# Kernel optimization log

Hardware: AMD Instinct MI355X
Metric: run time of the kernel (lower is better)

## Reference

```python
import jax, jax.numpy as jnp
import numpy as np
from functools import partial

B, DIN, H, D, HW = 4096, 2048, 1024, 256, 256
MAX_STEPS = 15
STEP = 1.0 / MAX_STEPS
WEIGHT = 1.0


def safe_norm(x):
    # per-sample L2 norm, keepdims, nan-safe at 0
    return jnp.sqrt(jnp.sum(x * x, axis=-1, keepdims=True) + 1e-24)


def setup_inputs() -> dict:
    key = jax.random.key(0)
    ks = jax.random.split(key, 16)
    s = lambda fan: 1.0 / np.sqrt(fan)
    inp = {
        'x_start': jax.random.normal(ks[0], (B, DIN), jnp.float32),
        'x_end': jax.random.normal(ks[1], (B, DIN), jnp.float32),
        'noise_raw': jax.random.normal(ks[2], (B, D), jnp.float32),
        # encoder params
        'W1': jax.random.normal(ks[3], (DIN, H), jnp.float32) * s(DIN),
        'b1': jnp.zeros((H,), jnp.float32),
        'W2': jax.random.normal(ks[4], (H, D), jnp.float32) * s(H),
        'b2': jnp.zeros((D,), jnp.float32),
        # Zermelo wind field params
        'Ww1': jax.random.normal(ks[5], (D, HW), jnp.float32) * s(D),
        'bw1': jnp.zeros((HW,), jnp.float32),
        'Ww2': jax.random.normal(ks[6], (HW, D), jnp.float32) * s(HW),
        'bw2': jnp.zeros((D,), jnp.float32),
        # conformal potential phi params (metric g = exp(phi) I)
        'Wp1': jax.random.normal(ks[7], (D, HW), jnp.float32) * s(D),
        'bp1': jnp.zeros((HW,), jnp.float32),
        'wp2': jax.random.normal(ks[8], (HW,), jnp.float32) * s(HW),
    }
    return inp


def _encode(x, W1, b1, W2, b2):
    return jnp.tanh(x @ W1 + b1) @ W2 + b2  # [B, D]


def _wind(z, Ww1, bw1, Ww2, bw2):
    return jnp.tanh(z @ Ww1 + bw1) @ Ww2 + bw2  # [B, D]


def _grad_phi(x, Wp1, bp1, wp2):
    # phi(x) = wp2 . tanh(x @ Wp1 + bp1); analytic gradient, fully vectorized
    h = jnp.tanh(x @ Wp1 + bp1)          # [B, HW]
    return ((1.0 - h * h) * wp2) @ Wp1.T  # [B, D]


def _accel(x, v, Wp1, bp1, wp2):
    # geodesic spray of conformal metric e^{phi} I:
    # a = -(grad_phi . v) v + 0.5 |v|^2 grad_phi
    g = _grad_phi(x, Wp1, bp1, wp2)
    gv = jnp.sum(g * v, axis=-1, keepdims=True)
    vv = jnp.sum(v * v, axis=-1, keepdims=True)
    return -gv * v + 0.5 * vv * g


def _trace(z0, v0, Wp1, bp1, wp2):
    h = STEP
    acc = partial(_accel, Wp1=Wp1, bp1=bp1, wp2=wp2)

    def step(carry, _):
        x, v = carry
        k1x, k1v = v, acc(x, v)
        k2x, k2v = v + 0.5 * h * k1v, acc(x + 0.5 * h * k1x, v + 0.5 * h * k1v)
        k3x, k3v = v + 0.5 * h * k2v, acc(x + 0.5 * h * k2x, v + 0.5 * h * k2v)
        k4x, k4v = v + h * k3v, acc(x + h * k3x, v + h * k3v)
        xn = x + (h / 6.0) * (k1x + 2 * k2x + 2 * k3x + k4x)
        vn = v + (h / 6.0) * (k1v + 2 * k2v + 2 * k3v + k4v)
        return (xn, vn), xn

    (_, _), xs = jax.lax.scan(step, (z0, v0), None, length=MAX_STEPS)
    return xs  # [MAX_STEPS, B, D] == xs[1:] of the original trace


def reference(x_start, x_end, noise_raw, W1, b1, W2, b2,
              Ww1, bw1, Ww2, bw2, Wp1, bp1, wp2):
    z_s = _encode(x_start, W1, b1, W2, b2)
    z_e = _encode(x_end, W1, b1, W2, b2)
    W_start = _wind(z_s, Ww1, bw1, Ww2, bw2)
    # degenerate-wind fallback: tiny tangent noise (Euclidean manifold -> identity projection)
    noise = noise_raw / (safe_norm(noise_raw) + 1e-12) * 1e-4
    w_norm = safe_norm(W_start)  # [B, 1]
    W_start = jnp.where(w_norm < 1e-5, W_start + noise, W_start)
    xs = _trace(z_s, W_start, Wp1, bp1, wp2)          # [S, B, D]
    dists_sq = jnp.sum((xs - z_e) ** 2, axis=-1)      # [S, B]
    min_dist_sq = jnp.min(dists_sq, axis=0)           # closest approach per sample
    return jnp.mean(min_dist_sq) * WEIGHT
```

## Files before the change

### kernel.cpp

```cpp
#include <hip/hip_runtime.h>
#include <math.h>

typedef short bf8 __attribute__((ext_vector_type(8)));
typedef float f32x4 __attribute__((ext_vector_type(4)));

namespace {

constexpr float H_STEP = 1.0f / 15.0f;

__device__ inline short f2bf(float f) {
  unsigned u = __float_as_uint(f);
  u += 0x7fffu + ((u >> 16) & 1u);
  return (short)(u >> 16);
}

__device__ inline float fast_tanh(float x) {
  const float ax = fabsf(x);
  const float e = __expf(-2.0f * ax);
  const float t = (1.0f - e) * __builtin_amdgcn_rcpf(1.0f + e);
  return copysignf(t, x);
}

__device__ inline float sech2(float x) {
  const float e = __expf(-2.0f * fabsf(x));
  const float r = __builtin_amdgcn_rcpf(1.0f + e);
  return 4.0f * e * r * r;
}

__device__ inline float wave_sum(float v) {
#pragma unroll
  for (int sh = 32; sh > 0; sh >>= 1) v += __shfl_xor(v, sh);
  return v;
}

template <int CTRL>
__device__ inline float dppadd(float v) {
  return v + __int_as_float(__builtin_amdgcn_update_dpp(
                 0, __float_as_int(v), CTRL, 0xF, 0xF, true));
}
__device__ inline float red16(float v) {
  v = dppadd<0x121>(v);
  v = dppadd<0x122>(v);
  v = dppadd<0x124>(v);
  v = dppadd<0x128>(v);
  return v;
}

__device__ inline void async16(const void* g, void* l) {
  __builtin_amdgcn_global_load_lds((__attribute__((address_space(1))) void*)g,
                                   (__attribute__((address_space(3))) void*)l,
                                   16, 0, 0);
}

__global__ __launch_bounds__(256) void prep_all(
    const float* __restrict__ xs, const float* __restrict__ xe,
    const float* __restrict__ W1, const float* __restrict__ W2,
    const float* __restrict__ Ww1, const float* __restrict__ Ww2,
    const float* __restrict__ Wp1, const float* __restrict__ wp2,
    short* __restrict__ XSb, short* __restrict__ W1T, short* __restrict__ W2T,
    short* __restrict__ Ww1T, short* __restrict__ Ww2T,
    short* __restrict__ WpT, short* __restrict__ Wp1s) {
  __shared__ float tile[32][33];
  const int id = blockIdx.x;
  if (id < 2048) {
    const long n = (long)8192 * 2048, half = n >> 1;
    long i = ((long)id * 256 + threadIdx.x) * 4;
    const long stride = (long)2048 * 1024;
    for (; i < n; i += stride) {
      const float* s = (i < half) ? (xs + i) : (xe + (i - half));
      const float4 f = *(const float4*)s;
      ushort4 o;
      o.x = (unsigned short)f2bf(f.x);
      o.y = (unsigned short)f2bf(f.y);
      o.z = (unsigned short)f2bf(f.z);
      o.w = (unsigned short)f2bf(f.w);
      *(ushort4*)(XSb + i) = o;
    }
    return;
  }
  const int tr = threadIdx.x >> 5, tc = threadIdx.x & 31;
  const float* src;
  short* dst;
  int K, N, kt, nt;
  if (id < 4096) {
    src = W1; dst = W1T; K = 2048; N = 1024; kt = (id - 2048) >> 5; nt = (id - 2048) & 31;
  } else if (id < 4352) {
    src = W2; dst = W2T; K = 1024; N = 256; kt = (id - 4096) >> 3; nt = (id - 4096) & 7;
  } else if (id < 4416) {
    src = Ww1; dst = Ww1T; K = 256; N = 256; kt = (id - 4352) >> 3; nt = (id - 4352) & 7;
  } else if (id < 4480) {
    src = Ww2; dst = Ww2T; K = 256; N = 256; kt = (id - 4416) >> 3; nt = (id - 4416) & 7;
  } else if (id < 4544) {
    src = Wp1; dst = WpT; K = 256; N = 256; kt = (id - 4480) >> 3; nt = (id - 4480) & 7;
  } else {
    const int lid = id - 4544;
    const int k0 = (lid >> 3) * 32, n0 = (lid & 7) * 32;
#pragma unroll
    for (int i = 0; i < 32; i += 8) {
      const size_t o = (size_t)(k0 + tr + i) * 256 + n0 + tc;
      Wp1s[o] = f2bf(Wp1[o] * wp2[n0 + tc]);
    }
    return;
  }
  const int k0 = kt * 32, n0 = nt * 32;
#pragma unroll
  for (int i = 0; i < 32; i += 8)
    tile[tr + i][tc] = src[(size_t)(k0 + tr + i) * N + n0 + tc];
  __syncthreads();
#pragma unroll
  for (int i = 0; i < 32; i += 8)
    dst[(size_t)(n0 + tr + i) * K + k0 + tc] = f2bf(tile[tc][tr + i]);
}


__global__ __launch_bounds__(256) void gemm128_tanh(
    const short* __restrict__ A, const short* __restrict__ Bt,
    const float* __restrict__ bias, short* __restrict__ Cb, int M, int N,
    int K) {
  __shared__ __align__(16) short As[2 * 128 * 32];
  __shared__ __align__(16) short Bs[2 * 128 * 32];
  const int tid = threadIdx.x;
  const int w = tid >> 6, lane = tid & 63, q = lane >> 4, l15 = lane & 15;
  const int wm = (w >> 1) * 64, wn = (w & 1) * 64;
  const int m0 = blockIdx.y * 128, n0 = blockIdx.x * 128;
  const f32x4 fzero = {0.0f, 0.0f, 0.0f, 0.0f};
  f32x4 acc[4][4];
#pragma unroll
  for (int mt = 0; mt < 4; ++mt)
#pragma unroll
    for (int nt = 0; nt < 4; ++nt) acc[mt][nt] = fzero;

  for (int k0 = 0; k0 < K; k0 += 64) {
#pragma unroll
    for (int kcb = 0; kcb < 2; ++kcb)
#pragma unroll
      for (int j = 0; j < 2; ++j) {
        const int c = w * 128 + j * 64 + lane;
        async16(A + (size_t)(m0 + (c >> 2)) * K + k0 + kcb * 32 + (c & 3) * 8,
                &As[kcb * 4096 + (w * 128 + j * 64) * 8]);
        async16(Bt + (size_t)(n0 + (c >> 2)) * K + k0 + kcb * 32 + (c & 3) * 8,
                &Bs[kcb * 4096 + (w * 128 + j * 64) * 8]);
      }
    __syncthreads();
#pragma unroll
    for (int kcb = 0; kcb < 2; ++kcb) {
      bf8 af[4], bfr[4];
#pragma unroll
      for (int mt = 0; mt < 4; ++mt)
        af[mt] =
            *(const bf8*)&As[kcb * 4096 + (wm + mt * 16 + l15) * 32 + q * 8];
#pragma unroll
      for (int nt = 0; nt < 4; ++nt)
        bfr[nt] =
            *(const bf8*)&Bs[kcb * 4096 + (wn + nt * 16 + l15) * 32 + q * 8];
#pragma unroll
      for (int mt = 0; mt < 4; ++mt)
#pragma unroll
        for (int nt = 0; nt < 4; ++nt)
          acc[mt][nt] = __builtin_amdgcn_mfma_f32_16x16x32_bf16(
              af[mt], bfr[nt], acc[mt][nt], 0, 0, 0);
    }
    __syncthreads();
  }
#pragma unroll
  for (int mt = 0; mt < 4; ++mt)
#pragma unroll
    for (int nt = 0; nt < 4; ++nt) {
      const int col = n0 + wn + nt * 16 + l15;
      const float bcol = bias[col];
#pragma unroll
      for (int rg = 0; rg < 4; ++rg) {
        const int row = m0 + wm + mt * 16 + q * 4 + rg;
        Cb[(size_t)row * N + col] = f2bf(fast_tanh(acc[mt][nt][rg] + bcol));
      }
    }
}

__global__ __launch_bounds__(256) void gemm64_enc2(
    const short* __restrict__ A, const short* __restrict__ Bt,
    const float* __restrict__ bias, float* __restrict__ Zs,
    float* __restrict__ Ze, int M, int N, int K) {
  __shared__ __align__(16) short As[2 * 64 * 32];
  __shared__ __align__(16) short Bs[2 * 64 * 32];
  const int tid = threadIdx.x;
  const int w = tid >> 6, lane = tid & 63, q = lane >> 4, l15 = lane & 15;
  const int wm = (w >> 1) * 32, wn = (w & 1) * 32;
  const int m0 = blockIdx.y * 64, n0 = blockIdx.x * 64;
  const f32x4 fzero = {0.0f, 0.0f, 0.0f, 0.0f};
  f32x4 acc[2][2];
#pragma unroll
  for (int mt = 0; mt < 2; ++mt)
#pragma unroll
    for (int nt = 0; nt < 2; ++nt) acc[mt][nt] = fzero;

  for (int k0 = 0; k0 < K; k0 += 64) {
    const int c = w * 64 + lane;
#pragma unroll
    for (int kcb = 0; kcb < 2; ++kcb) {
      async16(A + (size_t)(m0 + (c >> 2)) * K + k0 + kcb * 32 + (c & 3) * 8,
              &As[kcb * 2048 + (w * 64) * 8]);
      async16(Bt + (size_t)(n0 + (c >> 2)) * K + k0 + kcb * 32 + (c & 3) * 8,
              &Bs[kcb * 2048 + (w * 64) * 8]);
    }
    __syncthreads();
#pragma unroll
    for (int kcb = 0; kcb < 2; ++kcb) {
      bf8 af[2], bfr[2];
#pragma unroll
      for (int mt = 0; mt < 2; ++mt)
        af[mt] =
            *(const bf8*)&As[kcb * 2048 + (wm + mt * 16 + l15) * 32 + q * 8];
#pragma unroll
      for (int nt = 0; nt < 2; ++nt)
        bfr[nt] =
            *(const bf8*)&Bs[kcb * 2048 + (wn + nt * 16 + l15) * 32 + q * 8];
#pragma unroll
      for (int mt = 0; mt < 2; ++mt)
#pragma unroll
        for (int nt = 0; nt < 2; ++nt)
          acc[mt][nt] = __builtin_amdgcn_mfma_f32_16x16x32_bf16(
              af[mt], bfr[nt], acc[mt][nt], 0, 0, 0);
    }
    __syncthreads();
  }
#pragma unroll
  for (int mt = 0; mt < 2; ++mt)
#pragma unroll
    for (int nt = 0; nt < 2; ++nt) {
      const int col = n0 + wn + nt * 16 + l15;
      const float bcol = bias[col];
#pragma unroll
      for (int rg = 0; rg < 4; ++rg) {
        const int row = m0 + wm + mt * 16 + q * 4 + rg;
        const float val = acc[mt][nt][rg] + bcol;
        if (row < 4096)
          Zs[(size_t)row * N + col] = val;
        else
          Ze[(size_t)(row - 4096) * N + col] = val;
      }
    }
}


__global__ __launch_bounds__(512, 2) void trace_fused(
    const float* __restrict__ Xg, const float* __restrict__ ZEg,
    const float* __restrict__ NZg, const short* __restrict__ WT,
    const short* __restrict__ Wp1s, const short* __restrict__ Ww1T,
    const short* __restrict__ Ww2T, const float* __restrict__ bw1,
    const float* __restrict__ bw2, const float* __restrict__ bp1,
    float* __restrict__ out) {
  constexpr float hs = H_STEP;
  __shared__ __align__(16) short XsL[4096];
  __shared__ __align__(16) short UL[4096];
  __shared__ __align__(16) float gvb[2][16];
  __shared__ __align__(16) float vvb[2][16];
  __shared__ __align__(16) float db[2][16];
  const int tid = threadIdx.x;
  const int w = tid >> 6, lane = tid & 63, q = lane >> 4, l15 = lane & 15;
  const int r0 = blockIdx.x * 16, rb = q * 4;

  if (tid < 16) {
    gvb[0][tid] = 0.0f; gvb[1][tid] = 0.0f;
    vvb[0][tid] = 0.0f; vvb[1][tid] = 0.0f;
    db[0][tid] = 0.0f;  db[1][tid] = 0.0f;
  }

  int cc[2], wadr[2][4], radr[8];
  float bp1c[2], bw1c[2], bw2c[2];
#pragma unroll
  for (int t = 0; t < 2; ++t) {
    const int c = w * 32 + t * 16 + l15;
    cc[t] = c;
    const int kc = c >> 3, cx = kc & 15, cl = c & 7;
#pragma unroll
    for (int rg = 0; rg < 4; ++rg)
      wadr[t][rg] = kc * 128 + ((rb + rg) ^ cx) * 8 + cl;
    bp1c[t] = bp1[c];
    bw1c[t] = bw1[c];
    bw2c[t] = bw2[c];
  }
#pragma unroll
  for (int ks = 0; ks < 8; ++ks) {
    const int kq = ks * 4 + q;
    radr[ks] = (kq * 16 + (l15 ^ (kq & 15))) * 8;
  }
  float x[2][4], ze[2][4], nz[2][4];
#pragma unroll
  for (int t = 0; t < 2; ++t)
#pragma unroll
    for (int rg = 0; rg < 4; ++rg) {
      const size_t off = (size_t)(r0 + rb + rg) * 256 + cc[t];
      x[t][rg] = Xg[off];
      ze[t][rg] = ZEg[off];
      nz[t][rg] = NZg[off];
    }
  const f32x4 fzero = {0.0f, 0.0f, 0.0f, 0.0f};

  float v[2][4];
  {
    bf8 Wf1[2][8], Wf2[2][8];
#pragma unroll
    for (int t = 0; t < 2; ++t)
#pragma unroll
      for (int ks = 0; ks < 8; ++ks) {
        Wf1[t][ks] = *(const bf8*)(Ww1T + cc[t] * 256 + ks * 32 + q * 8);
        Wf2[t][ks] = *(const bf8*)(Ww2T + cc[t] * 256 + ks * 32 + q * 8);
      }
#pragma unroll
    for (int t = 0; t < 2; ++t)
#pragma unroll
      for (int rg = 0; rg < 4; ++rg) XsL[wadr[t][rg]] = f2bf(x[t][rg]);
    __syncthreads();
    bf8 af[8];
#pragma unroll
    for (int ks = 0; ks < 8; ++ks) af[ks] = *(const bf8*)&XsL[radr[ks]];
    f32x4 acc[2];
#pragma unroll
    for (int t = 0; t < 2; ++t) {
      f32x4 a0 = fzero, a1 = fzero;
#pragma unroll
      for (int ks = 0; ks < 8; ks += 2) {
        a0 = __builtin_amdgcn_mfma_f32_16x16x32_bf16(af[ks], Wf1[t][ks], a0,
                                                     0, 0, 0);
        a1 = __builtin_amdgcn_mfma_f32_16x16x32_bf16(af[ks + 1],
                                                     Wf1[t][ks + 1], a1, 0, 0,
                                                     0);
      }
      acc[t] = a0 + a1;
    }
#pragma unroll
    for (int t = 0; t < 2; ++t)
#pragma unroll
      for (int rg = 0; rg < 4; ++rg)
        UL[wadr[t][rg]] = f2bf(fast_tanh(acc[t][rg] + bw1c[t]));
    __syncthreads();
#pragma unroll
    for (int ks = 0; ks < 8; ++ks) af[ks] = *(const bf8*)&UL[radr[ks]];
#pragma unroll
    for (int t = 0; t < 2; ++t) {
      f32x4 a0 = fzero, a1 = fzero;
#pragma unroll
      for (int ks = 0; ks < 8; ks += 2) {
        a0 = __builtin_amdgcn_mfma_f32_16x16x32_bf16(af[ks], Wf2[t][ks], a0,
                                                     0, 0, 0);
        a1 = __builtin_amdgcn_mfma_f32_16x16x32_bf16(af[ks + 1],
                                                     Wf2[t][ks + 1], a1, 0, 0,
                                                     0);
      }
      acc[t] = a0 + a1;
#pragma unroll
      for (int rg = 0; rg < 4; ++rg) v[t][rg] = acc[t][rg] + bw2c[t];
    }
    float pn[4], pm[4];
#pragma unroll
    for (int rg = 0; rg < 4; ++rg) {
      pn[rg] = red16(v[0][rg] * v[0][rg] + v[1][rg] * v[1][rg]);
      pm[rg] = red16(nz[0][rg] * nz[0][rg] + nz[1][rg] * nz[1][rg]);
    }
    if (l15 == 0) {
#pragma unroll
      for (int rg = 0; rg < 4; ++rg) {
        atomicAdd(&gvb[0][rb + rg], pn[rg]);
        atomicAdd(&vvb[0][rb + rg], pm[rg]);
      }
    }
    __syncthreads();
#pragma unroll
    for (int rg = 0; rg < 4; ++rg) {
      const float wn = sqrtf(gvb[0][rb + rg] + 1e-24f);
      const float sc = (wn < 1e-5f)
                           ? 1e-4f / (sqrtf(vvb[0][rb + rg] + 1e-24f) + 1e-12f)
                           : 0.0f;
      v[0][rg] = fmaf(sc, nz[0][rg], v[0][rg]);
      v[1][rg] = fmaf(sc, nz[1][rg], v[1][rg]);
    }
    __syncthreads();
    if (tid < 16) {
      gvb[0][tid] = 0.0f;
      vvb[0][tid] = 0.0f;
    }
    __syncthreads();
  }

  bf8 B1f[2][8], B2f[2][8];
#pragma unroll
  for (int t = 0; t < 2; ++t)
#pragma unroll
    for (int ks = 0; ks < 8; ++ks) {
      B1f[t][ks] = *(const bf8*)(WT + cc[t] * 256 + ks * 32 + q * 8);
      B2f[t][ks] = *(const bf8*)(Wp1s + cc[t] * 256 + ks * 32 + q * 8);
    }
  float ap[2][4], xacc[2][4], vacc[2][4], md[4];
#pragma unroll
  for (int rg = 0; rg < 4; ++rg) {
    ap[0][rg] = 0.0f; ap[1][rg] = 0.0f;
    xacc[0][rg] = 0.0f; xacc[1][rg] = 0.0f;
    vacc[0][rg] = 0.0f; vacc[1][rg] = 0.0f;
    md[rg] = 3.4e38f;
  }
  const float cxv_t[4] = {0.0f, 0.5f * hs, 0.5f * hs, hs};
  const float cxa_t[4] = {0.0f, 0.0f, 0.25f * hs * hs, 0.5f * hs * hs};
  const float cva_t[4] = {0.0f, 0.5f * hs, 0.5f * hs, hs};

#pragma unroll 1
  for (int step = 0; step < 15; ++step) {
#pragma unroll
    for (int st = 0; st < 4; ++st) {
      const int p = st & 1;
      const float cxv = cxv_t[st], cxa = cxa_t[st], cva = cva_t[st];
      float vs[2][4];
#pragma unroll
      for (int t = 0; t < 2; ++t)
#pragma unroll
        for (int rg = 0; rg < 4; ++rg) {
          vs[t][rg] = fmaf(cva, ap[t][rg], v[t][rg]);
          XsL[wadr[t][rg]] =
              f2bf(x[t][rg] + cxv * v[t][rg] + cxa * ap[t][rg]);
        }
      {
        float pv[4];
#pragma unroll
        for (int rg = 0; rg < 4; ++rg)
          pv[rg] = red16(fmaf(vs[0][rg], vs[0][rg], vs[1][rg] * vs[1][rg]));
        if (l15 == 0) {
#pragma unroll
          for (int rg = 0; rg < 4; ++rg) atomicAdd(&vvb[p][rb + rg], pv[rg]);
        }
      }
      __syncthreads();
      if (st == 0 && step > 0) {
        const f32x4 d4 = *(const f32x4*)&db[(step - 1) & 1][rb];
#pragma unroll
        for (int rg = 0; rg < 4; ++rg) md[rg] = fminf(md[rg], d4[rg]);
      }
      bf8 af[8];
#pragma unroll
      for (int ks = 0; ks < 8; ++ks) af[ks] = *(const bf8*)&XsL[radr[ks]];
      f32x4 acc[2];
#pragma unroll
      for (int t = 0; t < 2; ++t) {
        f32x4 a0 = fzero, a1 = fzero;
#pragma unroll
        for (int ks = 0; ks < 8; ks += 2) {
          a0 = __builtin_amdgcn_mfma_f32_16x16x32_bf16(af[ks], B1f[t][ks], a0,
                                                       0, 0, 0);
          a1 = __builtin_amdgcn_mfma_f32_16x16x32_bf16(af[ks + 1],
                                                       B1f[t][ks + 1], a1, 0,
                                                       0, 0);
        }
        acc[t] = a0 + a1;
      }
#pragma unroll
      for (int t = 0; t < 2; ++t)
#pragma unroll
        for (int rg = 0; rg < 4; ++rg)
          UL[wadr[t][rg]] = f2bf(sech2(acc[t][rg] + bp1c[t]));
      if (tid < 16) {
        gvb[p ^ 1][tid] = 0.0f;
        vvb[p ^ 1][tid] = 0.0f;
      }
      __syncthreads();
      if (st == 0 && step > 0 && tid < 16) db[(step - 1) & 1][tid] = 0.0f;
#pragma unroll
      for (int ks = 0; ks < 8; ++ks) af[ks] = *(const bf8*)&UL[radr[ks]];
#pragma unroll
      for (int t = 0; t < 2; ++t) {
        f32x4 a0 = fzero, a1 = fzero;
#pragma unroll
        for (int ks = 0; ks < 8; ks += 2) {
          a0 = __builtin_amdgcn_mfma_f32_16x16x32_bf16(af[ks], B2f[t][ks], a0,
                                                       0, 0, 0);
          a1 = __builtin_amdgcn_mfma_f32_16x16x32_bf16(af[ks + 1],
                                                       B2f[t][ks + 1], a1, 0,
                                                       0, 0);
        }
        acc[t] = a0 + a1;
      }
      {
        float pg[4];
#pragma unroll
        for (int rg = 0; rg < 4; ++rg)
          pg[rg] =
              red16(fmaf(acc[0][rg], vs[0][rg], acc[1][rg] * vs[1][rg]));
        if (l15 == 0) {
#pragma unroll
          for (int rg = 0; rg < 4; ++rg) atomicAdd(&gvb[p][rb + rg], pg[rg]);
        }
      }
      __syncthreads();
      const f32x4 gv4 = *(const f32x4*)&gvb[p][rb];
      const f32x4 vv4 = *(const f32x4*)&vvb[p][rb];
#pragma unroll
      for (int t = 0; t < 2; ++t)
#pragma unroll
        for (int rg = 0; rg < 4; ++rg) {
          const float a = -gv4[rg] * vs[t][rg] + 0.5f * vv4[rg] * acc[t][rg];
          ap[t][rg] = a;
          if (st == 0) {
            xacc[t][rg] = a;
            vacc[t][rg] = a;
          } else if (st < 3) {
            xacc[t][rg] += a;
            vacc[t][rg] += 2.0f * a;
          } else {
            vacc[t][rg] += a;
          }
        }
      if (st == 3) {
        const int sp = step & 1;
        float pd[4];
#pragma unroll
        for (int rg = 0; rg < 4; ++rg) {
          float acc_d = 0.0f;
#pragma unroll
          for (int t = 0; t < 2; ++t) {
            const float xn =
                x[t][rg] + hs * v[t][rg] + (hs * hs / 6.0f) * xacc[t][rg];
            const float vn = v[t][rg] + (hs / 6.0f) * vacc[t][rg];
            x[t][rg] = xn;
            v[t][rg] = vn;
            const float d = xn - ze[t][rg];
            acc_d = fmaf(d, d, acc_d);
          }
          pd[rg] = red16(acc_d);
        }
        if (l15 == 0) {
#pragma unroll
          for (int rg = 0; rg < 4; ++rg) atomicAdd(&db[sp][rb + rg], pd[rg]);
        }
      }
    }
  }
  __syncthreads();
  {
    const f32x4 d4 = *(const f32x4*)&db[14 & 1][rb];
#pragma unroll
    for (int rg = 0; rg < 4; ++rg) md[rg] = fminf(md[rg], d4[rg]);
  }
  if (w == 0 && l15 == 0)
    atomicAdd(out, (md[0] + md[1] + md[2] + md[3]) * (1.0f / 4096.0f));
}

}

extern "C" void kernel_launch(void* const* d_in, const int* in_sizes, int n_in,
                              void* d_out, int out_size, void* d_ws,
                              size_t ws_size, hipStream_t stream) {
  (void)in_sizes; (void)n_in; (void)out_size; (void)ws_size;
  const float* x_start = (const float*)d_in[0];
  const float* x_end = (const float*)d_in[1];
  const float* noise = (const float*)d_in[2];
  const float* W1 = (const float*)d_in[3];
  const float* b1 = (const float*)d_in[4];
  const float* W2 = (const float*)d_in[5];
  const float* b2 = (const float*)d_in[6];
  const float* Ww1 = (const float*)d_in[7];
  const float* bw1 = (const float*)d_in[8];
  const float* Ww2 = (const float*)d_in[9];
  const float* bw2 = (const float*)d_in[10];
  const float* Wp1 = (const float*)d_in[11];
  const float* bp1 = (const float*)d_in[12];
  const float* wp2 = (const float*)d_in[13];
  float* out = (float*)d_out;

  float* Xf = (float*)d_ws;
  float* ZEf = Xf + (size_t)4096 * 256;
  short* XSb = (short*)(ZEf + (size_t)4096 * 256);
  short* H1b = XSb + (size_t)8192 * 2048;
  short* W1T = H1b + (size_t)8192 * 1024;
  short* W2T = W1T + (size_t)1024 * 2048;
  short* Ww1T = W2T + (size_t)256 * 1024;
  short* Ww2T = Ww1T + 65536;
  short* WpT = Ww2T + 65536;
  short* Wp1s = WpT + 65536;

  const dim3 blk(256);

  prep_all<<<4608, blk, 0, stream>>>(x_start, x_end, W1, W2, Ww1, Ww2, Wp1,
                                     wp2, XSb, W1T, W2T, Ww1T, Ww2T, WpT,
                                     Wp1s);
  gemm128_tanh<<<dim3(8, 64), blk, 0, stream>>>(XSb, W1T, b1, H1b, 8192, 1024,
                                                2048);
  gemm64_enc2<<<dim3(4, 128), blk, 0, stream>>>(H1b, W2T, b2, Xf, ZEf, 8192,
                                                256, 1024);
  hipMemsetAsync(d_out, 0, sizeof(float), stream);
  trace_fused<<<256, dim3(512), 0, stream>>>(Xf, ZEf, noise, WpT, Wp1s, Ww1T,
                                             Ww2T, bw1, bw2, bp1, out);
}
```

Before: 325.2 us.

## Halve rows per trace block and double grid; merge reductions and move min update

Each trace_fused block now handles 8 real rows instead of 16. Rows 8-15 are masked padding, and the grid doubles to 512 blocks so more CUs get work during the sequential RK4 loop. The vs/vv reduction moves after the second MFMA and merges with the gv reduction, which removes one red16+atomic phase before the first barrier. The per-step min-distance update moves inside step 3 with an extra barrier, and one redundant barrier is dropped. Half the MFMA work per block is wasted on zero rows, trading compute efficiency for parallelism on 256 CUs.

```diff
diff --git a/kernel.cpp b/kernel.cpp
--- a/kernel.cpp
+++ b/kernel.cpp
@@ -25,12 +25,6 @@
   const float e = __expf(-2.0f * fabsf(x));
   const float r = __builtin_amdgcn_rcpf(1.0f + e);
   return 4.0f * e * r * r;
-}
-
-__device__ inline float wave_sum(float v) {
-#pragma unroll
-  for (int sh = 32; sh > 0; sh >>= 1) v += __shfl_xor(v, sh);
-  return v;
 }
 
 template <int CTRL>
@@ -257,7 +251,8 @@
   __shared__ __align__(16) float db[2][16];
   const int tid = threadIdx.x;
   const int w = tid >> 6, lane = tid & 63, q = lane >> 4, l15 = lane & 15;
-  const int r0 = blockIdx.x * 16, rb = q * 4;
+  const int r0 = blockIdx.x * 8, rb = q * 4;
+  const float valid = (q < 2) ? 1.0f : 0.0f;
 
   if (tid < 16) {
     gvb[0][tid] = 0.0f; gvb[1][tid] = 0.0f;
@@ -289,10 +284,10 @@
   for (int t = 0; t < 2; ++t)
 #pragma unroll
     for (int rg = 0; rg < 4; ++rg) {
-      const size_t off = (size_t)(r0 + rb + rg) * 256 + cc[t];
-      x[t][rg] = Xg[off];
-      ze[t][rg] = ZEg[off];
-      nz[t][rg] = NZg[off];
+      const size_t off = (size_t)(r0 + ((rb + rg) & 7)) * 256 + cc[t];
+      x[t][rg] = Xg[off] * valid;
+      ze[t][rg] = ZEg[off] * valid;
+      nz[t][rg] = NZg[off] * valid;
     }
   const f32x4 fzero = {0.0f, 0.0f, 0.0f, 0.0f};
 
@@ -357,7 +352,7 @@
       pn[rg] = red16(v[0][rg] * v[0][rg] + v[1][rg] * v[1][rg]);
       pm[rg] = red16(nz[0][rg] * nz[0][rg] + nz[1][rg] * nz[1][rg]);
     }
-    if (l15 == 0) {
+    if (l15 == 0 && q < 2) {
 #pragma unroll
       for (int rg = 0; rg < 4; ++rg) {
         atomicAdd(&gvb[0][rb + rg], pn[rg]);
@@ -371,15 +366,14 @@
       const float sc = (wn < 1e-5f)
                            ? 1e-4f / (sqrtf(vvb[0][rb + rg] + 1e-24f) + 1e-12f)
                            : 0.0f;
-      v[0][rg] = fmaf(sc, nz[0][rg], v[0][rg]);
-      v[1][rg] = fmaf(sc, nz[1][rg], v[1][rg]);
+      v[0][rg] = fmaf(sc, nz[0][rg], v[0][rg]) * valid;
+      v[1][rg] = fmaf(sc, nz[1][rg], v[1][rg]) * valid;
     }
     __syncthreads();
     if (tid < 16) {
       gvb[0][tid] = 0.0f;
       vvb[0][tid] = 0.0f;
     }
-    __syncthreads();
   }
 
   bf8 B1f[2][8], B2f[2][8];
@@ -408,31 +402,13 @@
     for (int st = 0; st < 4; ++st) {
       const int p = st & 1;
       const float cxv = cxv_t[st], cxa = cxa_t[st], cva = cva_t[st];
-      float vs[2][4];
 #pragma unroll
       for (int t = 0; t < 2; ++t)
 #pragma unroll
-        for (int rg = 0; rg < 4; ++rg) {
-          vs[t][rg] = fmaf(cva, ap[t][rg], v[t][rg]);
+        for (int rg = 0; rg < 4; ++rg)
           XsL[wadr[t][rg]] =
               f2bf(x[t][rg] + cxv * v[t][rg] + cxa * ap[t][rg]);
-        }
-      {
-        float pv[4];
-#pragma unroll
-        for (int rg = 0; rg < 4; ++rg)
-          pv[rg] = red16(fmaf(vs[0][rg], vs[0][rg], vs[1][rg] * vs[1][rg]));
-        if (l15 == 0) {
-#pragma unroll
-          for (int rg = 0; rg < 4; ++rg) atomicAdd(&vvb[p][rb + rg], pv[rg]);
-        }
-      }
       __syncthreads();
-      if (st == 0 && step > 0) {
-        const f32x4 d4 = *(const f32x4*)&db[(step - 1) & 1][rb];
-#pragma unroll
-        for (int rg = 0; rg < 4; ++rg) md[rg] = fminf(md[rg], d4[rg]);
-      }
       bf8 af[8];
 #pragma unroll
       for (int ks = 0; ks < 8; ++ks) af[ks] = *(const bf8*)&XsL[radr[ks]];
@@ -454,13 +430,12 @@
       for (int t = 0; t < 2; ++t)
 #pragma unroll
         for (int rg = 0; rg < 4; ++rg)
-          UL[wadr[t][rg]] = f2bf(sech2(acc[t][rg] + bp1c[t]));
+          UL[wadr[t][rg]] = f2bf(sech2(acc[t][rg] + bp1c[t]) * valid);
       if (tid < 16) {
         gvb[p ^ 1][tid] = 0.0f;
         vvb[p ^ 1][tid] = 0.0f;
       }
       __syncthreads();
-      if (st == 0 && step > 0 && tid < 16) db[(step - 1) & 1][tid] = 0.0f;
 #pragma unroll
       for (int ks = 0; ks < 8; ++ks) af[ks] = *(const bf8*)&UL[radr[ks]];
 #pragma unroll
@@ -476,15 +451,19 @@
         }
         acc[t] = a0 + a1;
       }
-      {
-        float pg[4];
-#pragma unroll
-        for (int rg = 0; rg < 4; ++rg)
-          pg[rg] =
-              red16(fmaf(acc[0][rg], vs[0][rg], acc[1][rg] * vs[1][rg]));
-        if (l15 == 0) {
-#pragma unroll
-          for (int rg = 0; rg < 4; ++rg) atomicAdd(&gvb[p][rb + rg], pg[rg]);
+      float vs[2][4], pg[4], pv[4];
+#pragma unroll
+      for (int rg = 0; rg < 4; ++rg) {
+        vs[0][rg] = fmaf(cva, ap[0][rg], v[0][rg]);
+        vs[1][rg] = fmaf(cva, ap[1][rg], v[1][rg]);
+        pg[rg] = red16(fmaf(acc[0][rg], vs[0][rg], acc[1][rg] * vs[1][rg]));
+        pv[rg] = red16(fmaf(vs[0][rg], vs[0][rg], vs[1][rg] * vs[1][rg]));
+      }
+      if (l15 == 0 && q < 2) {
+#pragma unroll
+        for (int rg = 0; rg < 4; ++rg) {
+          atomicAdd(&gvb[p][rb + rg], pg[rg]);
+          atomicAdd(&vvb[p][rb + rg], pv[rg]);
         }
       }
       __syncthreads();
@@ -524,20 +503,19 @@
           }
           pd[rg] = red16(acc_d);
         }
-        if (l15 == 0) {
+        if (l15 == 0 && q < 2) {
 #pragma unroll
           for (int rg = 0; rg < 4; ++rg) atomicAdd(&db[sp][rb + rg], pd[rg]);
         }
-      }
-    }
-  }
-  __syncthreads();
-  {
-    const f32x4 d4 = *(const f32x4*)&db[14 & 1][rb];
-#pragma unroll
-    for (int rg = 0; rg < 4; ++rg) md[rg] = fminf(md[rg], d4[rg]);
-  }
-  if (w == 0 && l15 == 0)
+        if (tid < 16) db[sp ^ 1][tid] = 0.0f;
+        __syncthreads();
+        const f32x4 d4 = *(const f32x4*)&db[sp][rb];
+#pragma unroll
+        for (int rg = 0; rg < 4; ++rg) md[rg] = fminf(md[rg], d4[rg]);
+      }
+    }
+  }
+  if (w == 0 && l15 == 0 && q < 2)
     atomicAdd(out, (md[0] + md[1] + md[2] + md[3]) * (1.0f / 4096.0f));
 }
 
@@ -584,6 +562,6 @@
   gemm64_enc2<<<dim3(4, 128), blk, 0, stream>>>(H1b, W2T, b2, Xf, ZEf, 8192,
                                                 256, 1024);
   hipMemsetAsync(d_out, 0, sizeof(float), stream);
-  trace_fused<<<256, dim3(512), 0, stream>>>(Xf, ZEf, noise, WpT, Wp1s, Ww1T,
+  trace_fused<<<512, dim3(512), 0, stream>>>(Xf, ZEf, noise, WpT, Wp1s, Ww1T,
                                              Ww2T, bw1, bw2, bp1, out);
 }
```

After: 433.9 us. 33.4% more time.
